# Performance work log

Measured on AMD Instinct MI355X. Metric: run time of the kernel, lower is better.

Reference implementation:

```python
import jax, jax.numpy as jnp
import numpy as np

B = 4096        # graphs per batch
N_PER = 64      # nodes per graph
N = B * N_PER   # total nodes
D = 512         # embed_dim
T = 2048        # target_size


def setup_inputs() -> dict:
    key = jax.random.key(0)
    k1, k2, k3 = jax.random.split(key, 3)
    batch_emb = jax.random.normal(k1, (N, D), dtype=jnp.float32)
    # sorted per-node graph ids (PyG `batch` vector), all graphs non-empty
    seg = jnp.repeat(jnp.arange(B, dtype=jnp.int64), N_PER)
    # local node indices of the two query nodes in each graph
    targets = jax.random.randint(k2, (B, 2), 0, N_PER, dtype=jnp.int64)
    W = jax.random.normal(k3, (T, 3 * D), dtype=jnp.float32) * (1.0 / np.sqrt(3 * D))
    b = jnp.zeros((T,), dtype=jnp.float32)
    return {"batch_emb": batch_emb, "seg": seg, "targets": targets, "W": W, "b": b}


def reference(batch_emb, seg, targets, W, b):
    # per-graph mean pooling (segment mean)
    sums = jax.ops.segment_sum(batch_emb, seg, num_segments=B)          # [B, D]
    counts = jax.ops.segment_sum(jnp.ones((batch_emb.shape[0],), batch_emb.dtype),
                                 seg, num_segments=B)                   # [B]
    node_avg = sums / counts[:, None]                                   # [B, D]
    # convert local query indices to global node indices via segment starts
    starts = jnp.cumsum(counts.astype(jnp.int64)) - counts.astype(jnp.int64)  # [B]
    global_idx = starts[:, None] + targets                              # [B, 2]
    q = batch_emb[global_idx]                                           # [B, 2, D]
    final_embs = jnp.concatenate([q[:, 0], q[:, 1], node_avg], axis=-1) # [B, 3D]
    return final_embs @ W.T + b                                         # [B, T]
```

## Files before the change

kernel.cpp:

```cpp
#include <hip/hip_runtime.h>
#include <hip/hip_bf16.h>
#include <stdint.h>

#define B_GRAPHS 4096
#define N_PER    64
#define D_EMB    512
#define T_OUT    2048
#define K_DIM    1536
#define KT_N     (K_DIM/64)
#define WCONV_BLOCKS 512

typedef __bf16 bf16x8 __attribute__((ext_vector_type(8)));
typedef float  f32x4  __attribute__((ext_vector_type(4)));

__global__ __launch_bounds__(128) void pool_conv_kernel(
    const float* __restrict__ emb, const int* __restrict__ targets,
    const float* __restrict__ W,
    __hip_bfloat16* __restrict__ lhs, __hip_bfloat16* __restrict__ wb)
{
    union Pack { __hip_bfloat16 h[4]; uint2 u; };

    if (blockIdx.x >= B_GRAPHS) {
        const int total = T_OUT * K_DIM / 4;
        const int nthr  = WCONV_BLOCKS * 128;
        for (int i = (blockIdx.x - B_GRAPHS) * 128 + threadIdx.x;
             i < total; i += nthr) {
            const float4 v = reinterpret_cast<const float4*>(W)[i];
            Pack p;
            p.h[0] = __float2bfloat16(v.x); p.h[1] = __float2bfloat16(v.y);
            p.h[2] = __float2bfloat16(v.z); p.h[3] = __float2bfloat16(v.w);
            reinterpret_cast<uint2*>(wb)[i] = p.u;
        }
        return;
    }

    const int g = blockIdx.x;
    const int t = threadIdx.x;
    const int t0 = targets[2*g];
    const int t1 = targets[2*g + 1];
    const float4* rows = reinterpret_cast<const float4*>(emb)
                         + (size_t)g * N_PER * (D_EMB/4) + t;
    float4 acc = make_float4(0.f, 0.f, 0.f, 0.f);
    #pragma unroll 16
    for (int n = 0; n < N_PER; ++n) {
        float4 v = rows[(size_t)n * (D_EMB/4)];
        acc.x += v.x; acc.y += v.y; acc.z += v.z; acc.w += v.w;
    }
    const float s = 1.0f / (float)N_PER;
    float4 avg = make_float4(acc.x*s, acc.y*s, acc.z*s, acc.w*s);
    float4 q0 = rows[(size_t)t0 * (D_EMB/4)];
    float4 q1 = rows[(size_t)t1 * (D_EMB/4)];

    __hip_bfloat16* row = lhs + (size_t)g * K_DIM;
    Pack p0, p1, pa;
    p0.h[0] = __float2bfloat16(q0.x); p0.h[1] = __float2bfloat16(q0.y);
    p0.h[2] = __float2bfloat16(q0.z); p0.h[3] = __float2bfloat16(q0.w);
    p1.h[0] = __float2bfloat16(q1.x); p1.h[1] = __float2bfloat16(q1.y);
    p1.h[2] = __float2bfloat16(q1.z); p1.h[3] = __float2bfloat16(q1.w);
    pa.h[0] = __float2bfloat16(avg.x); pa.h[1] = __float2bfloat16(avg.y);
    pa.h[2] = __float2bfloat16(avg.z); pa.h[3] = __float2bfloat16(avg.w);
    reinterpret_cast<uint2*>(row)[t]             = p0.u;
    reinterpret_cast<uint2*>(row + D_EMB)[t]     = p1.u;
    reinterpret_cast<uint2*>(row + 2*D_EMB)[t]   = pa.u;
}

__global__ __launch_bounds__(256) void gemm_kernel(
    const __hip_bfloat16* __restrict__ A,
    const __hip_bfloat16* __restrict__ Bm,
    const float* __restrict__ bias,
    float* __restrict__ C)
{
    __shared__ __align__(16) __hip_bfloat16 As[2][128*64];
    __shared__ __align__(16) __hip_bfloat16 Bs[2][128*64];

    const int tid = threadIdx.x;
    const int w   = tid >> 6;
    const int l   = tid & 63;
    const int wr  = w >> 1;
    const int wc  = w & 1;
    const int brow = blockIdx.y * 128;
    const int bcol = blockIdx.x * 128;

    const int sr   = l >> 3;
    const int scol = 8 * ((l & 7) ^ sr);

    f32x4 acc[4][4];
    #pragma unroll
    for (int m = 0; m < 4; ++m)
        #pragma unroll
        for (int n = 0; n < 4; ++n)
            acc[m][n] = (f32x4){0.f, 0.f, 0.f, 0.f};

    const __hip_bfloat16* gA = A  + (size_t)(brow + w*32 + sr) * K_DIM + scol;
    const __hip_bfloat16* gB = Bm + (size_t)(bcol + w*32 + sr) * K_DIM + scol;

    auto stage = [&](int buf, int kt) {
        const int k0 = kt * 64;
        char* AsB = reinterpret_cast<char*>(As[buf]);
        char* BsB = reinterpret_cast<char*>(Bs[buf]);
        #pragma unroll
        for (int c = 0; c < 4; ++c) {
            const int ch = w * 4 + c;
            __builtin_amdgcn_global_load_lds(
                (const __attribute__((address_space(1))) void*)(gA + (size_t)c*8*K_DIM + k0),
                (__attribute__((address_space(3))) void*)(AsB + ch*1024), 16, 0, 0);
            __builtin_amdgcn_global_load_lds(
                (const __attribute__((address_space(1))) void*)(gB + (size_t)c*8*K_DIM + k0),
                (__attribute__((address_space(3))) void*)(BsB + ch*1024), 16, 0, 0);
        }
    };

    stage(0, 0);
    __syncthreads();

    int cur = 0;
    for (int kt = 0; kt < KT_N; ++kt) {
        if (kt + 1 < KT_N) stage(cur ^ 1, kt + 1);

        const char* AsB = reinterpret_cast<const char*>(As[cur]);
        const char* BsB = reinterpret_cast<const char*>(Bs[cur]);
        #pragma unroll
        for (int kk = 0; kk < 2; ++kk) {
            const int kbyte = kk*64 + (l >> 4)*16;
            bf16x8 af[4], bf[4];
            #pragma unroll
            for (int m = 0; m < 4; ++m) {
                const int r = wr*64 + m*16 + (l & 15);
                af[m] = *reinterpret_cast<const bf16x8*>(
                            AsB + r*128 + (kbyte ^ ((r & 7) << 4)));
            }
            #pragma unroll
            for (int n = 0; n < 4; ++n) {
                const int r = wc*64 + n*16 + (l & 15);
                bf[n] = *reinterpret_cast<const bf16x8*>(
                            BsB + r*128 + (kbyte ^ ((r & 7) << 4)));
            }
            #pragma unroll
            for (int m = 0; m < 4; ++m)
                #pragma unroll
                for (int n = 0; n < 4; ++n)
                    acc[m][n] = __builtin_amdgcn_mfma_f32_16x16x32_bf16(
                                    af[m], bf[n], acc[m][n], 0, 0, 0);
        }

        if (kt + 1 < KT_N) {
            __syncthreads();
            cur ^= 1;
        }
    }

    #pragma unroll
    for (int n = 0; n < 4; ++n) {
        const int col = bcol + wc*64 + n*16 + (l & 15);
        const float bv = bias[col];
        #pragma unroll
        for (int m = 0; m < 4; ++m) {
            const int row0 = brow + wr*64 + m*16 + (l >> 4)*4;
            #pragma unroll
            for (int e = 0; e < 4; ++e) {
                C[(size_t)(row0 + e) * T_OUT + col] = acc[m][n][e] + bv;
            }
        }
    }
}

extern "C" void kernel_launch(void* const* d_in, const int* in_sizes, int n_in,
                              void* d_out, int out_size, void* d_ws, size_t ws_size,
                              hipStream_t stream) {
    const float* emb     = (const float*)d_in[0];
    const int*   targets = (const int*)d_in[2];
    const float* W       = (const float*)d_in[3];
    const float* bias    = (const float*)d_in[4];
    float* out = (float*)d_out;

    __hip_bfloat16* lhs = (__hip_bfloat16*)d_ws;
    __hip_bfloat16* wb  = lhs + (size_t)B_GRAPHS * K_DIM;

    pool_conv_kernel<<<B_GRAPHS + WCONV_BLOCKS, 128, 0, stream>>>(
        emb, targets, W, lhs, wb);
    gemm_kernel<<<dim3(T_OUT/128, B_GRAPHS/128), 256, 0, stream>>>(lhs, wb, bias, out);
}
```

Baseline: 151.1 us.

## Fuse pooling and GEMM into one persistent kernel with flag-based round overlap

Merges the pooling/weight-conversion kernel and the GEMM into a single launch. 256 producer blocks convert W and pool graphs in 8 rounds, bumping per-round atomic counters. 256 GEMM blocks spin on those counters so each row band can start while later rows are still being pooled. This removes the kernel boundary and overlaps the memory-bound pooling with the MFMA GEMM. The cost is a memset, spin-wait overhead, fewer GEMM blocks each doing two tiles, and a risk of deadlock or stale data if producer and consumer blocks are not co-resident.

```diff
diff --git a/kernel.cpp b/kernel.cpp
--- a/kernel.cpp
+++ b/kernel.cpp
@@ -7,158 +7,176 @@
 #define D_EMB    512
 #define T_OUT    2048
 #define K_DIM    1536
-#define KT_N     (K_DIM/64)
-#define WCONV_BLOCKS 512
+#define KT_N     24
+#define NPOOL    256
+#define NGEMM    256
+#define ROUNDS   8
+#define CNT_OFF  (32u << 20)
 
 typedef __bf16 bf16x8 __attribute__((ext_vector_type(8)));
 typedef float  f32x4  __attribute__((ext_vector_type(4)));
 
-__global__ __launch_bounds__(128) void pool_conv_kernel(
+__global__ __launch_bounds__(256, 2) void fused_kernel(
     const float* __restrict__ emb, const int* __restrict__ targets,
-    const float* __restrict__ W,
-    __hip_bfloat16* __restrict__ lhs, __hip_bfloat16* __restrict__ wb)
-{
-    union Pack { __hip_bfloat16 h[4]; uint2 u; };
-
-    if (blockIdx.x >= B_GRAPHS) {
-        const int total = T_OUT * K_DIM / 4;
-        const int nthr  = WCONV_BLOCKS * 128;
-        for (int i = (blockIdx.x - B_GRAPHS) * 128 + threadIdx.x;
-             i < total; i += nthr) {
-            const float4 v = reinterpret_cast<const float4*>(W)[i];
-            Pack p;
-            p.h[0] = __float2bfloat16(v.x); p.h[1] = __float2bfloat16(v.y);
-            p.h[2] = __float2bfloat16(v.z); p.h[3] = __float2bfloat16(v.w);
-            reinterpret_cast<uint2*>(wb)[i] = p.u;
-        }
-        return;
-    }
-
-    const int g = blockIdx.x;
-    const int t = threadIdx.x;
-    const int t0 = targets[2*g];
-    const int t1 = targets[2*g + 1];
-    const float4* rows = reinterpret_cast<const float4*>(emb)
-                         + (size_t)g * N_PER * (D_EMB/4) + t;
-    float4 acc = make_float4(0.f, 0.f, 0.f, 0.f);
-    #pragma unroll 16
-    for (int n = 0; n < N_PER; ++n) {
-        float4 v = rows[(size_t)n * (D_EMB/4)];
-        acc.x += v.x; acc.y += v.y; acc.z += v.z; acc.w += v.w;
-    }
-    const float s = 1.0f / (float)N_PER;
-    float4 avg = make_float4(acc.x*s, acc.y*s, acc.z*s, acc.w*s);
-    float4 q0 = rows[(size_t)t0 * (D_EMB/4)];
-    float4 q1 = rows[(size_t)t1 * (D_EMB/4)];
-
-    __hip_bfloat16* row = lhs + (size_t)g * K_DIM;
-    Pack p0, p1, pa;
-    p0.h[0] = __float2bfloat16(q0.x); p0.h[1] = __float2bfloat16(q0.y);
-    p0.h[2] = __float2bfloat16(q0.z); p0.h[3] = __float2bfloat16(q0.w);
-    p1.h[0] = __float2bfloat16(q1.x); p1.h[1] = __float2bfloat16(q1.y);
-    p1.h[2] = __float2bfloat16(q1.z); p1.h[3] = __float2bfloat16(q1.w);
-    pa.h[0] = __float2bfloat16(avg.x); pa.h[1] = __float2bfloat16(avg.y);
-    pa.h[2] = __float2bfloat16(avg.z); pa.h[3] = __float2bfloat16(avg.w);
-    reinterpret_cast<uint2*>(row)[t]             = p0.u;
-    reinterpret_cast<uint2*>(row + D_EMB)[t]     = p1.u;
-    reinterpret_cast<uint2*>(row + 2*D_EMB)[t]   = pa.u;
-}
-
-__global__ __launch_bounds__(256) void gemm_kernel(
-    const __hip_bfloat16* __restrict__ A,
-    const __hip_bfloat16* __restrict__ Bm,
-    const float* __restrict__ bias,
-    float* __restrict__ C)
+    const float* __restrict__ W, const float* __restrict__ bias,
+    __hip_bfloat16* __restrict__ lhs, __hip_bfloat16* __restrict__ wb,
+    unsigned* __restrict__ cnt, float* __restrict__ C)
 {
     __shared__ __align__(16) __hip_bfloat16 As[2][128*64];
     __shared__ __align__(16) __hip_bfloat16 Bs[2][128*64];
 
-    const int tid = threadIdx.x;
-    const int w   = tid >> 6;
-    const int l   = tid & 63;
-    const int wr  = w >> 1;
-    const int wc  = w & 1;
-    const int brow = blockIdx.y * 128;
-    const int bcol = blockIdx.x * 128;
-
+    const int bid = blockIdx.x;
+    const int t   = threadIdx.x;
+    union Pack { __hip_bfloat16 h[4]; uint2 u; };
+
+    if (bid < NPOOL) {
+        {
+            const float4* Wf = reinterpret_cast<const float4*>(W);
+            #pragma unroll
+            for (int k2 = 0; k2 < 12; ++k2) {
+                const int i = bid*3072 + k2*256 + t;
+                const float4 v = Wf[i];
+                Pack p;
+                p.h[0] = __float2bfloat16(v.x); p.h[1] = __float2bfloat16(v.y);
+                p.h[2] = __float2bfloat16(v.z); p.h[3] = __float2bfloat16(v.w);
+                reinterpret_cast<uint2*>(wb)[i] = p.u;
+            }
+        }
+        __syncthreads();
+        if (t == 0)
+            __hip_atomic_fetch_add(&cnt[0], 1u, __ATOMIC_RELEASE, __HIP_MEMORY_SCOPE_AGENT);
+
+        const int s = t >> 7;
+        const int c = t & 127;
+        for (int r = 0; r < ROUNDS; ++r) {
+            const int g = 512*r + 2*bid + s;
+            const float4* gr = reinterpret_cast<const float4*>(emb)
+                               + (size_t)g * (N_PER * D_EMB/4) + c;
+            const int t0 = targets[2*g];
+            const int t1 = targets[2*g + 1];
+            float4 a = make_float4(0.f, 0.f, 0.f, 0.f);
+            #pragma unroll 16
+            for (int n = 0; n < N_PER; ++n) {
+                const float4 v = gr[(size_t)n * (D_EMB/4)];
+                a.x += v.x; a.y += v.y; a.z += v.z; a.w += v.w;
+            }
+            const float sc = 1.0f / (float)N_PER;
+            const float4 q0 = gr[(size_t)t0 * (D_EMB/4)];
+            const float4 q1 = gr[(size_t)t1 * (D_EMB/4)];
+            __hip_bfloat16* row = lhs + (size_t)g * K_DIM;
+            Pack p0, p1, pa;
+            p0.h[0] = __float2bfloat16(q0.x); p0.h[1] = __float2bfloat16(q0.y);
+            p0.h[2] = __float2bfloat16(q0.z); p0.h[3] = __float2bfloat16(q0.w);
+            p1.h[0] = __float2bfloat16(q1.x); p1.h[1] = __float2bfloat16(q1.y);
+            p1.h[2] = __float2bfloat16(q1.z); p1.h[3] = __float2bfloat16(q1.w);
+            pa.h[0] = __float2bfloat16(a.x*sc); pa.h[1] = __float2bfloat16(a.y*sc);
+            pa.h[2] = __float2bfloat16(a.z*sc); pa.h[3] = __float2bfloat16(a.w*sc);
+            reinterpret_cast<uint2*>(row)[c]           = p0.u;
+            reinterpret_cast<uint2*>(row + D_EMB)[c]   = p1.u;
+            reinterpret_cast<uint2*>(row + 2*D_EMB)[c] = pa.u;
+
+            __syncthreads();
+            if (t == 0)
+                __hip_atomic_fetch_add(&cnt[1+r], 1u, __ATOMIC_RELEASE, __HIP_MEMORY_SCOPE_AGENT);
+        }
+        return;
+    }
+
+    const int j  = bid - NPOOL;
+    const int w  = t >> 6, l = t & 63;
+    const int wr = w >> 1, wc = w & 1;
     const int sr   = l >> 3;
     const int scol = 8 * ((l & 7) ^ sr);
-
-    f32x4 acc[4][4];
-    #pragma unroll
-    for (int m = 0; m < 4; ++m)
+    const int bx   = j & 15;
+
+    for (int half = 0; half < 2; ++half) {
+        const int by = (j >> 4) + 16*half;
+        if (t == 0) {
+            volatile unsigned* flag = &cnt[1 + (by >> 2)];
+            int guard = 0;
+            while (__hip_atomic_load((const unsigned*)flag, __ATOMIC_ACQUIRE,
+                                     __HIP_MEMORY_SCOPE_AGENT) < (unsigned)NPOOL) {
+                __builtin_amdgcn_s_sleep(16);
+                if (++guard > (1 << 22)) break;
+            }
+        }
+        __syncthreads();
+
+        const int brow = by * 128, bcol = bx * 128;
+        f32x4 acc[4][4];
         #pragma unroll
-        for (int n = 0; n < 4; ++n)
-            acc[m][n] = (f32x4){0.f, 0.f, 0.f, 0.f};
-
-    const __hip_bfloat16* gA = A  + (size_t)(brow + w*32 + sr) * K_DIM + scol;
-    const __hip_bfloat16* gB = Bm + (size_t)(bcol + w*32 + sr) * K_DIM + scol;
-
-    auto stage = [&](int buf, int kt) {
-        const int k0 = kt * 64;
-        char* AsB = reinterpret_cast<char*>(As[buf]);
-        char* BsB = reinterpret_cast<char*>(Bs[buf]);
+        for (int m = 0; m < 4; ++m)
+            #pragma unroll
+            for (int n = 0; n < 4; ++n)
+                acc[m][n] = (f32x4){0.f, 0.f, 0.f, 0.f};
+
+        const __hip_bfloat16* gA = lhs + (size_t)(brow + w*32 + sr) * K_DIM + scol;
+        const __hip_bfloat16* gB = wb  + (size_t)(bcol + w*32 + sr) * K_DIM + scol;
+
+        auto stage = [&](int buf, int kt) {
+            const int k0 = kt * 64;
+            char* AsB = reinterpret_cast<char*>(As[buf]);
+            char* BsB = reinterpret_cast<char*>(Bs[buf]);
+            #pragma unroll
+            for (int cc = 0; cc < 4; ++cc) {
+                const int ch = w * 4 + cc;
+                __builtin_amdgcn_global_load_lds(
+                    (const __attribute__((address_space(1))) void*)(gA + (size_t)cc*8*K_DIM + k0),
+                    (__attribute__((address_space(3))) void*)(AsB + ch*1024), 16, 0, 0);
+                __builtin_amdgcn_global_load_lds(
+                    (const __attribute__((address_space(1))) void*)(gB + (size_t)cc*8*K_DIM + k0),
+                    (__attribute__((address_space(3))) void*)(BsB + ch*1024), 16, 0, 0);
+            }
+        };
+
+        stage(0, 0);
+        __syncthreads();
+
+        int cur = 0;
+        for (int kt = 0; kt < KT_N; ++kt) {
+            if (kt + 1 < KT_N) stage(cur ^ 1, kt + 1);
+            const char* AsB = reinterpret_cast<const char*>(As[cur]);
+            const char* BsB = reinterpret_cast<const char*>(Bs[cur]);
+            #pragma unroll
+            for (int kk = 0; kk < 2; ++kk) {
+                const int kbyte = kk*64 + (l >> 4)*16;
+                bf16x8 af[4], bf[4];
+                #pragma unroll
+                for (int m = 0; m < 4; ++m) {
+                    const int r = wr*64 + m*16 + (l & 15);
+                    af[m] = *reinterpret_cast<const bf16x8*>(
+                                AsB + r*128 + (kbyte ^ ((r & 7) << 4)));
+                }
+                #pragma unroll
+                for (int n = 0; n < 4; ++n) {
+                    const int r = wc*64 + n*16 + (l & 15);
+                    bf[n] = *reinterpret_cast<const bf16x8*>(
+                                BsB + r*128 + (kbyte ^ ((r & 7) << 4)));
+                }
+                #pragma unroll
+                for (int m = 0; m < 4; ++m)
+                    #pragma unroll
+                    for (int n = 0; n < 4; ++n)
+                        acc[m][n] = __builtin_amdgcn_mfma_f32_16x16x32_bf16(
+                                        af[m], bf[n], acc[m][n], 0, 0, 0);
+            }
+            if (kt + 1 < KT_N) {
+                __syncthreads();
+                cur ^= 1;
+            }
+        }
+
         #pragma unroll
-        for (int c = 0; c < 4; ++c) {
-            const int ch = w * 4 + c;
-            __builtin_amdgcn_global_load_lds(
-                (const __attribute__((address_space(1))) void*)(gA + (size_t)c*8*K_DIM + k0),
-                (__attribute__((address_space(3))) void*)(AsB + ch*1024), 16, 0, 0);
-            __builtin_amdgcn_global_load_lds(
-                (const __attribute__((address_space(1))) void*)(gB + (size_t)c*8*K_DIM + k0),
-                (__attribute__((address_space(3))) void*)(BsB + ch*1024), 16, 0, 0);
-        }
-    };
-
-    stage(0, 0);
-    __syncthreads();
-
-    int cur = 0;
-    for (int kt = 0; kt < KT_N; ++kt) {
-        if (kt + 1 < KT_N) stage(cur ^ 1, kt + 1);
-
-        const char* AsB = reinterpret_cast<const char*>(As[cur]);
-        const char* BsB = reinterpret_cast<const char*>(Bs[cur]);
-        #pragma unroll
-        for (int kk = 0; kk < 2; ++kk) {
-            const int kbyte = kk*64 + (l >> 4)*16;
-            bf16x8 af[4], bf[4];
+        for (int n = 0; n < 4; ++n) {
+            const int col = bcol + wc*64 + n*16 + (l & 15);
+            const float bv = bias[col];
             #pragma unroll
             for (int m = 0; m < 4; ++m) {
-                const int r = wr*64 + m*16 + (l & 15);
-                af[m] = *reinterpret_cast<const bf16x8*>(
-                            AsB + r*128 + (kbyte ^ ((r & 7) << 4)));
-            }
-            #pragma unroll
-            for (int n = 0; n < 4; ++n) {
-                const int r = wc*64 + n*16 + (l & 15);
-                bf[n] = *reinterpret_cast<const bf16x8*>(
-                            BsB + r*128 + (kbyte ^ ((r & 7) << 4)));
-            }
-            #pragma unroll
-            for (int m = 0; m < 4; ++m)
-                #pragma unroll
-                for (int n = 0; n < 4; ++n)
-                    acc[m][n] = __builtin_amdgcn_mfma_f32_16x16x32_bf16(
-                                    af[m], bf[n], acc[m][n], 0, 0, 0);
-        }
-
-        if (kt + 1 < KT_N) {
-            __syncthreads();
-            cur ^= 1;
-        }
-    }
-
-    #pragma unroll
-    for (int n = 0; n < 4; ++n) {
-        const int col = bcol + wc*64 + n*16 + (l & 15);
-        const float bv = bias[col];
-        #pragma unroll
-        for (int m = 0; m < 4; ++m) {
-            const int row0 = brow + wr*64 + m*16 + (l >> 4)*4;
-            #pragma unroll
-            for (int e = 0; e < 4; ++e) {
-                C[(size_t)(row0 + e) * T_OUT + col] = acc[m][n][e] + bv;
+                const int row0 = brow + wr*64 + m*16 + (l >> 4)*4;
+                #pragma unroll
+                for (int e = 0; e < 4; ++e) {
+                    C[(size_t)(row0 + e) * T_OUT + col] = acc[m][n][e] + bv;
+                }
             }
         }
     }
@@ -175,8 +193,10 @@
 
     __hip_bfloat16* lhs = (__hip_bfloat16*)d_ws;
     __hip_bfloat16* wb  = lhs + (size_t)B_GRAPHS * K_DIM;
-
-    pool_conv_kernel<<<B_GRAPHS + WCONV_BLOCKS, 128, 0, stream>>>(
-        emb, targets, W, lhs, wb);
-    gemm_kernel<<<dim3(T_OUT/128, B_GRAPHS/128), 256, 0, stream>>>(lhs, wb, bias, out);
+    unsigned* cnt = (unsigned*)((char*)d_ws + CNT_OFF);
+
+    hipMemsetAsync(cnt, 0, 256, stream);
+
+    fused_kernel<<<NPOOL + NGEMM, 256, 0, stream>>>(
+        emb, targets, W, bias, lhs, wb, cnt, out);
 }
```

Result: slower. 309.0 us (+104.4%).
